# Performance work log

Hardware: AMD Instinct MI355X
Metric: run time of the kernel (lower is better)

## Reference

```python
import jax, jax.numpy as jnp
import numpy as np

NEG_SLOPE = 0.2  # GAT LeakyReLU slope
NEG_INF = -1e9


def setup_inputs() -> dict:
    key = jax.random.key(0)
    ks = jax.random.split(key, 5)
    B, N, D = 16, 1024, 256
    H, F = 4, 64  # heads, per-head out dim (out_dim=256)
    x = jax.random.normal(ks[0], (B, N, D), dtype=jnp.float32)
    adj = jax.random.uniform(ks[1], (B, N, N), dtype=jnp.float32)
    W = jax.random.normal(ks[2], (D, H * F), dtype=jnp.float32) * (1.0 / np.sqrt(D))
    a_src = jax.random.normal(ks[3], (H, F), dtype=jnp.float32) * (1.0 / np.sqrt(F))
    a_dst = jax.random.normal(ks[4], (H, F), dtype=jnp.float32) * (1.0 / np.sqrt(F))
    bias = jnp.zeros((H * F,), dtype=jnp.float32)
    return {"x": x, "adj": adj, "W": W, "a_src": a_src, "a_dst": a_dst, "bias": bias}


def reference(x, adj, W, a_src, a_dst, bias):
    B, N, D = x.shape
    H, F = a_src.shape
    # Linear transform per head: [B,N,H,F]
    h = jnp.einsum("bnd,dhf->bnhf", x, W.reshape(D, H, F))
    # Attention logit components: [B,N,H]
    e_src = jnp.einsum("bnhf,hf->bnh", h, a_src)
    e_dst = jnp.einsum("bnhf,hf->bnh", h, a_dst)
    # logits[b,i,j,h]: target i gathers from source j (edge = adj[b,i,j] > 0.5)
    logits = e_dst[:, :, None, :] + e_src[:, None, :, :]
    logits = jnp.where(logits >= 0, logits, NEG_SLOPE * logits)  # LeakyReLU
    mask = adj > 0.5  # [B,N,N]
    logits = jnp.where(mask[..., None], logits, NEG_INF)
    att = jax.nn.softmax(logits, axis=2)  # softmax over source neighbors j
    out = jnp.einsum("bijh,bjhf->bihf", att, h)  # aggregate
    return out.reshape(B, N, H * F) + bias  # concat heads
```

## Files before the change

kernel.cpp:

```cpp
#include <hip/hip_runtime.h>

typedef __bf16 bf16x8 __attribute__((ext_vector_type(8)));
typedef float f32x4 __attribute__((ext_vector_type(4)));

constexpr int Bsz = 16;
constexpr int Nsz = 1024;
constexpr int Dsz = 256;
constexpr int Hsz = 4;
constexpr int HFsz = 256;
constexpr int BN = Bsz * Nsz;
constexpr float LOG2E = 1.44269504088896340736f;

__device__ __forceinline__ unsigned f2bf(float f) {
    unsigned u = __float_as_uint(f);
    return (u + 0x7FFFu + ((u >> 16) & 1u)) >> 16;
}

__global__ __launch_bounds__(256) void wcvt(const float* __restrict__ Wm,
                                            unsigned short* __restrict__ WbT) {
    const int t = threadIdx.x;
    const int c = blockIdx.x * 4 + (t >> 6);
    const int d0 = (t & 63) * 4;
    const float v0 = Wm[(size_t)(d0 + 0) * HFsz + c];
    const float v1 = Wm[(size_t)(d0 + 1) * HFsz + c];
    const float v2 = Wm[(size_t)(d0 + 2) * HFsz + c];
    const float v3 = Wm[(size_t)(d0 + 3) * HFsz + c];
    uint2 pk;
    pk.x = f2bf(v0) | (f2bf(v1) << 16);
    pk.y = f2bf(v2) | (f2bf(v3) << 16);
    *(uint2*)&WbT[(size_t)c * Dsz + d0] = pk;
}

__global__ __launch_bounds__(256) void adjbin(const float* __restrict__ adj,
                                              unsigned char* __restrict__ adjM) {
    const int wg = (blockIdx.x * 256 + threadIdx.x) >> 6;
    const int lane = threadIdx.x & 63;
#pragma unroll 1
    for (int s = wg; s < 32768; s += 2048) {
        const int r = s >> 1, c0 = (s & 1) * 512;
        const float4* src = (const float4*)(adj + (size_t)r * 1024 + c0 + lane * 8);
        const float4 a0 = src[0], a1 = src[1];
        unsigned by = 0;
        by |= (a0.x > 0.5f) ? 1u : 0u;
        by |= (a0.y > 0.5f) ? 2u : 0u;
        by |= (a0.z > 0.5f) ? 4u : 0u;
        by |= (a0.w > 0.5f) ? 8u : 0u;
        by |= (a1.x > 0.5f) ? 16u : 0u;
        by |= (a1.y > 0.5f) ? 32u : 0u;
        by |= (a1.z > 0.5f) ? 64u : 0u;
        by |= (a1.w > 0.5f) ? 128u : 0u;
        const int j8 = (s & 1) * 64 + lane;
        adjM[(size_t)(r >> 4) * 2048 + (j8 >> 3) * 128 + (r & 15) * 8 + (j8 & 7)] =
            (unsigned char)by;
    }
}

__global__ __launch_bounds__(256) void gat_h_e3(
    const float* __restrict__ x,
    const unsigned short* __restrict__ WbT,
    const float* __restrict__ a_src,
    const float* __restrict__ a_dst,
    unsigned short* __restrict__ hT,
    float* __restrict__ esrcT,
    float* __restrict__ edstT)
{
    const int n0g = blockIdx.x * 32, b = n0g >> 10, n0 = n0g & 1023;
    const int t = threadIdx.x, lane = t & 63, w = t >> 6;
    const int m = lane & 15, q = lane >> 4;

    __shared__ alignas(16) unsigned short Lds[4 * 64 * 40];

    const float4* x4 = (const float4*)(x + (size_t)n0g * Dsz);
#pragma unroll
    for (int i = 0; i < 8; ++i) {
        const int f = t + 256 * i;
        const int row = f >> 6, d4 = (f & 63) * 4;
        const float4 xv = x4[f];
        uint2 pk;
        pk.x = f2bf(xv.x) | (f2bf(xv.y) << 16);
        pk.y = f2bf(xv.z) | (f2bf(xv.w) << 16);
        *(uint2*)&Lds[row * 264 + d4] = pk;
    }
    __syncthreads();

    const unsigned short* Ab = WbT + (size_t)(w * 64 + m) * Dsz + q * 8;
    f32x4 acc[4][2];
#pragma unroll
    for (int ht = 0; ht < 4; ++ht)
#pragma unroll
        for (int nt = 0; nt < 2; ++nt) acc[ht][nt] = (f32x4){0.f, 0.f, 0.f, 0.f};

#pragma unroll
    for (int kk = 0; kk < 8; ++kk) {
        const int k0 = kk * 32;
        const bf16x8 bfr0 = *(const bf16x8*)&Lds[(0 * 16 + m) * 264 + k0 + q * 8];
        const bf16x8 bfr1 = *(const bf16x8*)&Lds[(1 * 16 + m) * 264 + k0 + q * 8];
#pragma unroll
        for (int ht = 0; ht < 4; ++ht) {
            const bf16x8 afr = *(const bf16x8*)&Ab[ht * 16 * Dsz + k0];
            acc[ht][0] = __builtin_amdgcn_mfma_f32_16x16x32_bf16(afr, bfr0, acc[ht][0], 0, 0, 0);
            acc[ht][1] = __builtin_amdgcn_mfma_f32_16x16x32_bf16(afr, bfr1, acc[ht][1], 0, 0, 0);
        }
    }

    float ps0 = 0.f, ps1 = 0.f, pd0 = 0.f, pd1 = 0.f;
#pragma unroll
    for (int ht = 0; ht < 4; ++ht)
#pragma unroll
        for (int r = 0; r < 4; ++r) {
            const float as = a_src[w * 64 + ht * 16 + q * 4 + r];
            const float ad = a_dst[w * 64 + ht * 16 + q * 4 + r];
            ps0 += acc[ht][0][r] * as;  ps1 += acc[ht][1][r] * as;
            pd0 += acc[ht][0][r] * ad;  pd1 += acc[ht][1][r] * ad;
        }
    ps0 += __shfl_xor(ps0, 16, 64); ps0 += __shfl_xor(ps0, 32, 64);
    ps1 += __shfl_xor(ps1, 16, 64); ps1 += __shfl_xor(ps1, 32, 64);
    pd0 += __shfl_xor(pd0, 16, 64); pd0 += __shfl_xor(pd0, 32, 64);
    pd1 += __shfl_xor(pd1, 16, 64); pd1 += __shfl_xor(pd1, 32, 64);
    if (q == 0) {
        const size_t eb = (size_t)(b * Hsz + w) * Nsz + n0;
        esrcT[eb + m]      = ps0 * LOG2E;  esrcT[eb + 16 + m] = ps1 * LOG2E;
        edstT[eb + m]      = pd0 * LOG2E;  edstT[eb + 16 + m] = pd1 * LOG2E;
    }

    __syncthreads();

#pragma unroll
    for (int ht = 0; ht < 4; ++ht)
#pragma unroll
        for (int r = 0; r < 4; ++r) {
            const int hf = ht * 16 + q * 4 + r;
            Lds[w * 2560 + hf * 40 + m]      = (unsigned short)f2bf(acc[ht][0][r]);
            Lds[w * 2560 + hf * 40 + 16 + m] = (unsigned short)f2bf(acc[ht][1][r]);
        }
#pragma unroll
    for (int s = 0; s < 4; ++s) {
        const int hf = s * 16 + (lane >> 2), ck = lane & 3;
        const bf16x8 hv = *(const bf16x8*)&Lds[w * 2560 + hf * 40 + ck * 8];
        *(bf16x8*)&hT[(size_t)(b * HFsz + w * 64 + hf) * Nsz + n0 + ck * 8] = hv;
    }
}

__global__ __launch_bounds__(128, 8) void gat_attn8(
    const unsigned char* __restrict__ adjM,
    const unsigned short* __restrict__ hT,
    const float* __restrict__ esrcT,
    const float* __restrict__ edstT,
    const float* __restrict__ bias,
    float* __restrict__ outp)
{
    const int gid = blockIdx.x;
    const int b  = gid & 15;
    const int hw = (gid >> 4) & 3;
    const int it = gid >> 6, i0 = it * 16;
    const int t = threadIdx.x;
    const int lane = t & 63, jh = t >> 6;
    const int m = lane & 15, q = lane >> 4;

    __shared__ alignas(16) float smem[2560];
    unsigned short* Pw = (unsigned short*)smem + jh * 1152;

    const float* esb = esrcT + (size_t)(b * Hsz + hw) * Nsz;
    const float* edb = edstT + (size_t)(b * Hsz + hw) * Nsz + i0;
    const unsigned short* hTb = hT + (size_t)(b * HFsz + hw * 64 + m) * Nsz + q * 8;
    const unsigned long long* mkb =
        (const unsigned long long*)(adjM + (size_t)(b * 64 + it) * 2048);

    float edv[16];
#pragma unroll
    for (int il = 0; il < 16; ++il)
        edv[il] = __uint_as_float(
            __builtin_amdgcn_readfirstlane(__float_as_uint(edb[il])));

    bf16x8 ones;
#pragma unroll
    for (int i = 0; i < 8; ++i)
        ((unsigned short*)&ones)[i] = 0x3F80;

    f32x4 acc[4];
#pragma unroll
    for (int nt = 0; nt < 4; ++nt) acc[nt] = (f32x4){0.f, 0.f, 0.f, 0.f};
    f32x4 acc5 = (f32x4){0.f, 0.f, 0.f, 0.f};

    const int jt0 = jh * 8;
    float esC = esb[jt0 * 64 + lane];

#pragma unroll 1
    for (int jl = 0; jl < 8; ++jl) {
        const int jt = jt0 + jl;
        const int j0 = jt * 64;
        const int jtu = __builtin_amdgcn_readfirstlane(jt);

        bf16x8 bfr0[4], bfr1[4];
#pragma unroll
        for (int nt = 0; nt < 4; ++nt)
            bfr0[nt] = *(const bf16x8*)&hTb[(size_t)nt * 16 * Nsz + j0];

        const int jn = (jl < 7) ? (j0 + 64) : j0;
        const float esN = esb[jn + lane];

        unsigned long long mk[16];
#pragma unroll
        for (int il = 0; il < 16; ++il) mk[il] = mkb[jtu * 16 + il];

#pragma unroll
        for (int il = 0; il < 16; ++il) {
            float v = edv[il] + esC;
            v = fmaxf(v, 0.2f * v);
            float p;
            asm("v_exp_f32 %0, %1" : "=v"(p) : "v"(v));
            unsigned ru;
            asm("v_cndmask_b32 %0, 0, %1, %2"
                : "=v"(ru) : "v"(p), "s"(mk[il]));
            Pw[il * 72 + lane] = (unsigned short)(ru >> 16);
        }

#pragma unroll
        for (int nt = 0; nt < 4; ++nt)
            bfr1[nt] = *(const bf16x8*)&hTb[(size_t)nt * 16 * Nsz + j0 + 32];

        {
            const bf16x8 af0 = *(const bf16x8*)&Pw[m * 72 + q * 8];
#pragma unroll
            for (int nt = 0; nt < 4; ++nt)
                acc[nt] = __builtin_amdgcn_mfma_f32_16x16x32_bf16(
                    af0, bfr0[nt], acc[nt], 0, 0, 0);
            acc5 = __builtin_amdgcn_mfma_f32_16x16x32_bf16(af0, ones, acc5, 0, 0, 0);
        }
        {
            const bf16x8 af1 = *(const bf16x8*)&Pw[m * 72 + 32 + q * 8];
#pragma unroll
            for (int nt = 0; nt < 4; ++nt)
                acc[nt] = __builtin_amdgcn_mfma_f32_16x16x32_bf16(
                    af1, bfr1[nt], acc[nt], 0, 0, 0);
            acc5 = __builtin_amdgcn_mfma_f32_16x16x32_bf16(af1, ones, acc5, 0, 0, 0);
        }
        esC = esN;
    }

    __syncthreads();
    {
        float* cw = smem + t * 20;
#pragma unroll
        for (int nt = 0; nt < 4; ++nt)
#pragma unroll
            for (int r = 0; r < 4; ++r) cw[nt * 4 + r] = acc[nt][r];
#pragma unroll
        for (int r = 0; r < 4; ++r) cw[16 + r] = acc5[r];
    }
    __syncthreads();

#pragma unroll
    for (int u = 0; u < 2; ++u) {
        const int idx = t * 2 + u;
        const int row = idx >> 4, c4 = idx & 15;
        const int rq = row >> 2, rr = row & 3;
        const int nt4 = (c4 >> 2) * 4, mb = (c4 & 3) * 4;
        float n0 = 0.f, n1 = 0.f, n2 = 0.f, n3 = 0.f, den = 0.f;
#pragma unroll
        for (int j2 = 0; j2 < 2; ++j2) {
            const float* cb = smem + (j2 * 64 + rq * 16) * 20;
            den += cb[16 + rr];
            n0 += cb[(mb + 0) * 20 + nt4 + rr];
            n1 += cb[(mb + 1) * 20 + nt4 + rr];
            n2 += cb[(mb + 2) * 20 + nt4 + rr];
            n3 += cb[(mb + 3) * 20 + nt4 + rr];
        }
        const float inv = 1.f / den;
        const float4 b4 = *(const float4*)&bias[hw * 64 + c4 * 4];
        float4 o;
        o.x = n0 * inv + b4.x;  o.y = n1 * inv + b4.y;
        o.z = n2 * inv + b4.z;  o.w = n3 * inv + b4.w;
        *(float4*)&outp[(size_t)(b * Nsz + i0 + row) * HFsz + hw * 64 + c4 * 4] = o;
    }
}

extern "C" void kernel_launch(void* const* d_in, const int* in_sizes, int n_in,
                              void* d_out, int out_size, void* d_ws, size_t ws_size,
                              hipStream_t stream) {
    const float* x     = (const float*)d_in[0];
    const float* adj   = (const float*)d_in[1];
    const float* Wm    = (const float*)d_in[2];
    const float* a_src = (const float*)d_in[3];
    const float* a_dst = (const float*)d_in[4];
    const float* bias  = (const float*)d_in[5];
    float* outp = (float*)d_out;

    unsigned short* hT  = (unsigned short*)d_ws;
    unsigned short* WbT = hT + (size_t)BN * HFsz;
    float* esrcT = (float*)(WbT + (size_t)HFsz * Dsz);
    float* edstT = esrcT + (size_t)Bsz * Hsz * Nsz;
    unsigned char* adjM = (unsigned char*)(edstT + (size_t)Bsz * Hsz * Nsz);

    adjbin<<<dim3(512), dim3(256), 0, stream>>>(adj, adjM);
    wcvt<<<dim3(64), dim3(256), 0, stream>>>(Wm, WbT);
    gat_h_e3<<<dim3(BN / 32), dim3(256), 0, stream>>>(x, WbT, a_src, a_dst,
                                                      hT, esrcT, edstT);
    gat_attn8<<<dim3(4096), dim3(128), 0, stream>>>(adjM, hT, esrcT, edstT,
                                                    bias, outp);
}
```

Measured before the change: 190.3 us.

## Double-buffer h tiles, masks and e_src across attention loop iterations

The attention kernel's j-loop now prefetches the next tile's hT fragments, adjacency mask words and e_src value into a second register set while the current tile runs its exp/mask and MFMA work. The loop is unrolled by two with ping-pong buffers. This is meant to hide global load latency behind compute. To make room for the extra registers, the launch bound's minimum blocks per CU is halved, so occupancy may drop.

```diff
diff --git a/kernel.cpp b/kernel.cpp
--- a/kernel.cpp
+++ b/kernel.cpp
@@ -141,7 +141,7 @@
     }
 }
 
-__global__ __launch_bounds__(128, 8) void gat_attn8(
+__global__ __launch_bounds__(128, 4) void gat_attn10(
     const unsigned char* __restrict__ adjM,
     const unsigned short* __restrict__ hT,
     const float* __restrict__ esrcT,
@@ -182,26 +182,33 @@
     for (int nt = 0; nt < 4; ++nt) acc[nt] = (f32x4){0.f, 0.f, 0.f, 0.f};
     f32x4 acc5 = (f32x4){0.f, 0.f, 0.f, 0.f};
 
-    const int jt0 = jh * 8;
-    float esC = esb[jt0 * 64 + lane];
-
-#pragma unroll 1
-    for (int jl = 0; jl < 8; ++jl) {
-        const int jt = jt0 + jl;
-        const int j0 = jt * 64;
-        const int jtu = __builtin_amdgcn_readfirstlane(jt);
-
-        bf16x8 bfr0[4], bfr1[4];
-#pragma unroll
-        for (int nt = 0; nt < 4; ++nt)
-            bfr0[nt] = *(const bf16x8*)&hTb[(size_t)nt * 16 * Nsz + j0];
-
-        const int jn = (jl < 7) ? (j0 + 64) : j0;
-        const float esN = esb[jn + lane];
-
-        unsigned long long mk[16];
-#pragma unroll
-        for (int il = 0; il < 16; ++il) mk[il] = mkb[jtu * 16 + il];
+    const int jt0 = __builtin_amdgcn_readfirstlane(jh * 8);
+
+    unsigned long long mkA[16], mkB[16];
+    bf16x8 bfA[8], bfB[8];
+    float esA, esB;
+#pragma unroll
+    for (int il = 0; il < 16; ++il) mkA[il] = mkb[jt0 * 16 + il];
+#pragma unroll
+    for (int nt = 0; nt < 4; ++nt) {
+        bfA[nt]     = *(const bf16x8*)&hTb[(size_t)nt * 16 * Nsz + jt0 * 64];
+        bfA[4 + nt] = *(const bf16x8*)&hTb[(size_t)nt * 16 * Nsz + jt0 * 64 + 32];
+    }
+    esA = esb[jt0 * 64 + lane];
+
+    auto body = [&](int jl, unsigned long long (&mkC)[16], bf16x8 (&bfC)[8],
+                    float& esC, unsigned long long (&mkN)[16], bf16x8 (&bfN)[8],
+                    float& esN) {
+        const int jnx = (jl < 7) ? (jt0 + jl + 1) : (jt0 + jl);
+        const int jnu = __builtin_amdgcn_readfirstlane(jnx);
+#pragma unroll
+        for (int nt = 0; nt < 4; ++nt) {
+            bfN[nt]     = *(const bf16x8*)&hTb[(size_t)nt * 16 * Nsz + jnx * 64];
+            bfN[4 + nt] = *(const bf16x8*)&hTb[(size_t)nt * 16 * Nsz + jnx * 64 + 32];
+        }
+        esN = esb[jnx * 64 + lane];
+#pragma unroll
+        for (int il = 0; il < 16; ++il) mkN[il] = mkb[jnu * 16 + il];
 
 #pragma unroll
         for (int il = 0; il < 16; ++il) {
@@ -211,20 +218,16 @@
             asm("v_exp_f32 %0, %1" : "=v"(p) : "v"(v));
             unsigned ru;
             asm("v_cndmask_b32 %0, 0, %1, %2"
-                : "=v"(ru) : "v"(p), "s"(mk[il]));
+                : "=v"(ru) : "v"(p), "s"(mkC[il]));
             Pw[il * 72 + lane] = (unsigned short)(ru >> 16);
         }
-
-#pragma unroll
-        for (int nt = 0; nt < 4; ++nt)
-            bfr1[nt] = *(const bf16x8*)&hTb[(size_t)nt * 16 * Nsz + j0 + 32];
 
         {
             const bf16x8 af0 = *(const bf16x8*)&Pw[m * 72 + q * 8];
 #pragma unroll
             for (int nt = 0; nt < 4; ++nt)
                 acc[nt] = __builtin_amdgcn_mfma_f32_16x16x32_bf16(
-                    af0, bfr0[nt], acc[nt], 0, 0, 0);
+                    af0, bfC[nt], acc[nt], 0, 0, 0);
             acc5 = __builtin_amdgcn_mfma_f32_16x16x32_bf16(af0, ones, acc5, 0, 0, 0);
         }
         {
@@ -232,10 +235,15 @@
 #pragma unroll
             for (int nt = 0; nt < 4; ++nt)
                 acc[nt] = __builtin_amdgcn_mfma_f32_16x16x32_bf16(
-                    af1, bfr1[nt], acc[nt], 0, 0, 0);
+                    af1, bfC[4 + nt], acc[nt], 0, 0, 0);
             acc5 = __builtin_amdgcn_mfma_f32_16x16x32_bf16(af1, ones, acc5, 0, 0, 0);
         }
-        esC = esN;
+    };
+
+#pragma unroll 1
+    for (int jp = 0; jp < 8; jp += 2) {
+        body(jp,     mkA, bfA, esA, mkB, bfB, esB);
+        body(jp + 1, mkB, bfB, esB, mkA, bfA, esA);
     }
 
     __syncthreads();
@@ -296,6 +304,6 @@
     wcvt<<<dim3(64), dim3(256), 0, stream>>>(Wm, WbT);
     gat_h_e3<<<dim3(BN / 32), dim3(256), 0, stream>>>(x, WbT, a_src, a_dst,
                                                       hT, esrcT, edstT);
-    gat_attn8<<<dim3(4096), dim3(128), 0, stream>>>(adjM, hT, esrcT, edstT,
-                                                    bias, outp);
-}
+    gat_attn10<<<dim3(4096), dim3(128), 0, stream>>>(adjM, hT, esrcT, edstT,
+                                                     bias, outp);
+}
```

Result: slower. 200.8 us (+5.5%).

## Build attention MFMA A-fragments in registers instead of via LDS

Applied to the files above, without the earlier changes.

Each lane now computes the exact probability values it needs for its own MFMA A-operand fragment (row m, columns q*8..q*8+7). It does this from a per-lane dst logit, vectorized src-logit loads and a per-row 64-bit mask, so the fragments are assembled directly in registers. This removes the LDS write/read round trip for P and the per-row scalar mask loads. In exchange each lane does redundant global loads of esrc and per-bit selects instead of SGPR cndmask, and launch bounds drop from 8 to 6 waves per SIMD target.

```diff
diff --git a/kernel.cpp b/kernel.cpp
--- a/kernel.cpp
+++ b/kernel.cpp
@@ -141,7 +141,7 @@
     }
 }
 
-__global__ __launch_bounds__(128, 8) void gat_attn8(
+__global__ __launch_bounds__(128, 6) void gat_attn11(
     const unsigned char* __restrict__ adjM,
     const unsigned short* __restrict__ hT,
     const float* __restrict__ esrcT,
@@ -158,19 +158,11 @@
     const int m = lane & 15, q = lane >> 4;
 
     __shared__ alignas(16) float smem[2560];
-    unsigned short* Pw = (unsigned short*)smem + jh * 1152;
 
     const float* esb = esrcT + (size_t)(b * Hsz + hw) * Nsz;
-    const float* edb = edstT + (size_t)(b * Hsz + hw) * Nsz + i0;
+    const float ed_s = edstT[(size_t)(b * Hsz + hw) * Nsz + i0 + m];
     const unsigned short* hTb = hT + (size_t)(b * HFsz + hw * 64 + m) * Nsz + q * 8;
-    const unsigned long long* mkb =
-        (const unsigned long long*)(adjM + (size_t)(b * 64 + it) * 2048);
-
-    float edv[16];
-#pragma unroll
-    for (int il = 0; il < 16; ++il)
-        edv[il] = __uint_as_float(
-            __builtin_amdgcn_readfirstlane(__float_as_uint(edb[il])));
+    const unsigned char* mkb = adjM + (size_t)(b * 64 + it) * 2048 + m * 8;
 
     bf16x8 ones;
 #pragma unroll
@@ -183,59 +175,79 @@
     f32x4 acc5 = (f32x4){0.f, 0.f, 0.f, 0.f};
 
     const int jt0 = jh * 8;
-    float esC = esb[jt0 * 64 + lane];
+    const int q8 = q * 8;
 
 #pragma unroll 1
     for (int jl = 0; jl < 8; ++jl) {
         const int jt = jt0 + jl;
         const int j0 = jt * 64;
-        const int jtu = __builtin_amdgcn_readfirstlane(jt);
-
+
+        const unsigned long long mk =
+            *(const unsigned long long*)(mkb + jt * 128);
         bf16x8 bfr0[4], bfr1[4];
 #pragma unroll
         for (int nt = 0; nt < 4; ++nt)
             bfr0[nt] = *(const bf16x8*)&hTb[(size_t)nt * 16 * Nsz + j0];
-
-        const int jn = (jl < 7) ? (j0 + 64) : j0;
-        const float esN = esb[jn + lane];
-
-        unsigned long long mk[16];
-#pragma unroll
-        for (int il = 0; il < 16; ++il) mk[il] = mkb[jtu * 16 + il];
-
-#pragma unroll
-        for (int il = 0; il < 16; ++il) {
-            float v = edv[il] + esC;
-            v = fmaxf(v, 0.2f * v);
-            float p;
-            asm("v_exp_f32 %0, %1" : "=v"(p) : "v"(v));
-            unsigned ru;
-            asm("v_cndmask_b32 %0, 0, %1, %2"
-                : "=v"(ru) : "v"(p), "s"(mk[il]));
-            Pw[il * 72 + lane] = (unsigned short)(ru >> 16);
+        const float4 e0a = *(const float4*)&esb[j0 + q8];
+        const float4 e0b = *(const float4*)&esb[j0 + q8 + 4];
+
+        const unsigned mlo = (unsigned)mk, mhi = (unsigned)(mk >> 32);
+        const unsigned by0 = mlo >> q8;
+
+        union { unsigned u[4]; bf16x8 v; } af0;
+        {
+            const float e[8] = {e0a.x, e0a.y, e0a.z, e0a.w,
+                                e0b.x, e0b.y, e0b.z, e0b.w};
+#pragma unroll
+            for (int r = 0; r < 4; ++r) {
+                float va = ed_s + e[2 * r], vb = ed_s + e[2 * r + 1];
+                va = fmaxf(va, 0.2f * va);
+                vb = fmaxf(vb, 0.2f * vb);
+                float pa, pb;
+                asm("v_exp_f32 %0, %1" : "=v"(pa) : "v"(va));
+                asm("v_exp_f32 %0, %1" : "=v"(pb) : "v"(vb));
+                const unsigned ua = ((by0 >> (2 * r)) & 1u) ? __float_as_uint(pa) : 0u;
+                const unsigned ub = ((by0 >> (2 * r + 1)) & 1u) ? __float_as_uint(pb) : 0u;
+                af0.u[r] = (ua >> 16) | (ub & 0xFFFF0000u);
+            }
         }
 
 #pragma unroll
         for (int nt = 0; nt < 4; ++nt)
             bfr1[nt] = *(const bf16x8*)&hTb[(size_t)nt * 16 * Nsz + j0 + 32];
-
+        const float4 e1a = *(const float4*)&esb[j0 + 32 + q8];
+        const float4 e1b = *(const float4*)&esb[j0 + 32 + q8 + 4];
+
+#pragma unroll
+        for (int nt = 0; nt < 4; ++nt)
+            acc[nt] = __builtin_amdgcn_mfma_f32_16x16x32_bf16(
+                af0.v, bfr0[nt], acc[nt], 0, 0, 0);
+        acc5 = __builtin_amdgcn_mfma_f32_16x16x32_bf16(af0.v, ones, acc5, 0, 0, 0);
+
+        union { unsigned u[4]; bf16x8 v; } af1;
         {
-            const bf16x8 af0 = *(const bf16x8*)&Pw[m * 72 + q * 8];
-#pragma unroll
-            for (int nt = 0; nt < 4; ++nt)
-                acc[nt] = __builtin_amdgcn_mfma_f32_16x16x32_bf16(
-                    af0, bfr0[nt], acc[nt], 0, 0, 0);
-            acc5 = __builtin_amdgcn_mfma_f32_16x16x32_bf16(af0, ones, acc5, 0, 0, 0);
-        }
-        {
-            const bf16x8 af1 = *(const bf16x8*)&Pw[m * 72 + 32 + q * 8];
-#pragma unroll
-            for (int nt = 0; nt < 4; ++nt)
-                acc[nt] = __builtin_amdgcn_mfma_f32_16x16x32_bf16(
-                    af1, bfr1[nt], acc[nt], 0, 0, 0);
-            acc5 = __builtin_amdgcn_mfma_f32_16x16x32_bf16(af1, ones, acc5, 0, 0, 0);
-        }
-        esC = esN;
+            const unsigned by1 = mhi >> q8;
+            const float e[8] = {e1a.x, e1a.y, e1a.z, e1a.w,
+                                e1b.x, e1b.y, e1b.z, e1b.w};
+#pragma unroll
+            for (int r = 0; r < 4; ++r) {
+                float va = ed_s + e[2 * r], vb = ed_s + e[2 * r + 1];
+                va = fmaxf(va, 0.2f * va);
+                vb = fmaxf(vb, 0.2f * vb);
+                float pa, pb;
+                asm("v_exp_f32 %0, %1" : "=v"(pa) : "v"(va));
+                asm("v_exp_f32 %0, %1" : "=v"(pb) : "v"(vb));
+                const unsigned ua = ((by1 >> (2 * r)) & 1u) ? __float_as_uint(pa) : 0u;
+                const unsigned ub = ((by1 >> (2 * r + 1)) & 1u) ? __float_as_uint(pb) : 0u;
+                af1.u[r] = (ua >> 16) | (ub & 0xFFFF0000u);
+            }
+        }
+
+#pragma unroll
+        for (int nt = 0; nt < 4; ++nt)
+            acc[nt] = __builtin_amdgcn_mfma_f32_16x16x32_bf16(
+                af1.v, bfr1[nt], acc[nt], 0, 0, 0);
+        acc5 = __builtin_amdgcn_mfma_f32_16x16x32_bf16(af1.v, ones, acc5, 0, 0, 0);
     }
 
     __syncthreads();
@@ -296,6 +308,6 @@
     wcvt<<<dim3(64), dim3(256), 0, stream>>>(Wm, WbT);
     gat_h_e3<<<dim3(BN / 32), dim3(256), 0, stream>>>(x, WbT, a_src, a_dst,
                                                       hT, esrcT, edstT);
-    gat_attn8<<<dim3(4096), dim3(128), 0, stream>>>(adjM, hT, esrcT, edstT,
-                                                    bias, outp);
-}
+    gat_attn11<<<dim3(4096), dim3(128), 0, stream>>>(adjM, hT, esrcT, edstT,
+                                                     bias, outp);
+}
```

Measured after the change: 199.1 us. +4.6%, slower.
